# Optimization experiments

Hardware: AMD Instinct MI355X
Metric: run time of the kernel (lower is better)

The kernel has to match this reference:

```python
import jax, jax.numpy as jnp
import numpy as np

BS, N, HD = 16, 96, 128      # batch, nodes per graph, hidden_nf
NL, NS = 4, 2                # n_layers, inv_sublayers
ND, HF = 3, 6                # n_dims, node feature dims (in_node_nf - time)
FIN = HF + 1                 # +1 time channel (condition_time=True)
NF = 100.0                   # normalization_factor, aggregation='sum'


def setup_inputs() -> dict:
    key = jax.random.key(0)
    ks = iter(jax.random.split(key, 40))

    def w(shape, scale=None):
        s = scale if scale is not None else 1.0 / np.sqrt(shape[-2])
        return jax.random.normal(next(ks), shape, jnp.float32) * s

    xh = jax.random.normal(next(ks), (BS, N, ND + HF), jnp.float32)
    t = jnp.array([0.5], jnp.float32)
    nm = (jax.random.uniform(next(ks), (BS, N, 1)) < 0.9).astype(jnp.float32)
    em = nm[:, :, None, :] * nm[:, None, :, :]
    em = em * (1.0 - jnp.eye(N, dtype=jnp.float32)[None, :, :, None])
    G = NL * NS
    return dict(
        xh=xh, t=t, node_mask=nm, edge_mask=em,
        W_emb=w((FIN, HD)), b_emb=jnp.zeros((HD,), jnp.float32),
        gWe1=w((G, 2 * HD + 2, HD)), gbe1=jnp.zeros((G, HD), jnp.float32),
        gWe2=w((G, HD, HD)), gbe2=jnp.zeros((G, HD), jnp.float32),
        gWn1=w((G, 2 * HD, HD)), gbn1=jnp.zeros((G, HD), jnp.float32),
        gWn2=w((G, HD, HD)), gbn2=jnp.zeros((G, HD), jnp.float32),
        eWc1=w((NL, 2 * HD + 2, HD)), ebc1=jnp.zeros((NL, HD), jnp.float32),
        eWc2=w((NL, HD, HD)), ebc2=jnp.zeros((NL, HD), jnp.float32),
        eWc3=w((NL, HD, 1), scale=0.001),   # xavier gain 0.001 as in EDM
        W_out=w((HD, FIN)), b_out=jnp.zeros((FIN,), jnp.float32),
    )


def _pair_mlp(h, ea, W1, b1, W2, b2):
    # silu(Linear(cat([h_i, h_j, ea]))) -> silu(Linear) without materializing the concat
    hi = h @ W1[:HD]            # (B,N,H) source part
    hj = h @ W1[HD:2 * HD]      # (B,N,H) target part
    m = jax.nn.silu(hi[:, :, None, :] + hj[:, None, :, :] + ea @ W1[2 * HD:] + b1)
    return jax.nn.silu(m @ W2 + b2)          # (B,N,N,H)


def _egnn(xh, t, node_mask, edge_mask, W_emb, b_emb, gWe1, gbe1, gWe2, gbe2,
          gWn1, gbn1, gWn2, gbn2, eWc1, ebc1, eWc2, ebc2, eWc3, W_out, b_out):
    xh = xh * node_mask                       # mask padded nodes
    x0 = xh[..., :ND]                         # (B,N,3)
    h_time = jnp.broadcast_to(t.reshape(1, 1, 1), (xh.shape[0], xh.shape[1], 1))
    h = jnp.concatenate([xh[..., ND:], h_time], axis=-1)   # (B,N,FIN)
    h = h @ W_emb + b_emb                     # node embedding
    # initial squared distances (EGNN-level edge_attr, in_edge_nf=1)
    d0 = jnp.sum((x0[:, :, None] - x0[:, None, :]) ** 2, -1, keepdims=True)
    x = x0
    for l in range(NL):                       # EquivariantBlocks
        diff = x[:, :, None] - x[:, None, :]  # x_i - x_j, (B,N,N,3)
        radial = jnp.sum(diff ** 2, -1, keepdims=True)
        coord_diff = diff / jnp.sqrt(radial + 1e-8)   # norm_constant=0
        ea = jnp.concatenate([radial, d0], axis=-1)   # (B,N,N,2)
        for s in range(NS):                   # GCL sublayers
            g = l * NS + s
            m = _pair_mlp(h, ea, gWe1[g], gbe1[g], gWe2[g], gbe2[g]) * edge_mask
            agg = jnp.sum(m, axis=2) / NF     # masked scatter-sum over j onto i
            u = jax.nn.silu(h @ gWn1[g, :HD] + agg @ gWn1[g, HD:] + gbn1[g])
            h = (h + (u @ gWn2[g] + gbn2[g])) * node_mask
        # EquivariantUpdate (tanh=False)
        phi = _pair_mlp(h, ea, eWc1[l], ebc1[l], eWc2[l], ebc2[l])
        trans = coord_diff * (phi @ eWc3[l]) * edge_mask    # (B,N,N,3)
        x = (x + jnp.sum(trans, axis=2) / NF) * node_mask
    h = (h @ W_out + b_out) * node_mask       # embedding_out
    vel = (x - x0) * node_mask
    # remove_mean_with_mask
    n_per = jnp.sum(node_mask, axis=1, keepdims=True)
    vel = vel - (jnp.sum(vel, axis=1, keepdims=True) / n_per) * node_mask
    # drop the appended time channel from h (condition_time=True, context=None)
    return jnp.concatenate([vel, h[..., :HF]], axis=-1)    # (B,N,3+HF)


def reference(xh, t, node_mask, edge_mask, W_emb, b_emb, gWe1, gbe1, gWe2, gbe2,
              gWn1, gbn1, gWn2, gbn2, eWc1, ebc1, eWc2, ebc2, eWc3, W_out, b_out):
    return _egnn(xh, t, node_mask, edge_mask, W_emb, b_emb, gWe1, gbe1, gWe2, gbe2,
                 gWn1, gbn1, gWn2, gbn2, eWc1, ebc1, eWc2, ebc2, eWc3, W_out, b_out)
```

## Files before the change

kernel.cpp:

```cpp
#include <hip/hip_runtime.h>
#include <hip/hip_bf16.h>

#define BSZ 16
#define Nn 96
#define HD 128
#define NDIM 3
#define HFEAT 6
#define FINC 7
#define BN (BSZ*Nn)

typedef const float* fp;
typedef __bf16 bf16x8_t __attribute__((ext_vector_type(8)));
typedef float  f32x4_t  __attribute__((ext_vector_type(4)));

__device__ __forceinline__ float silu(float x){
  float e = __expf(-x);
  return x * __builtin_amdgcn_rcpf(1.f + e);
}
__device__ __forceinline__ unsigned short f2b(float x){
  unsigned u = __float_as_uint(x);
  unsigned r = u + 0x7FFF + ((u>>16)&1);
  return (unsigned short)(r>>16);
}
__device__ __forceinline__ unsigned pkf(float a, float b){
  __hip_bfloat162 h2 = __float22bfloat162_rn(make_float2(a,b));
  return *reinterpret_cast<unsigned*>(&h2);
}


__global__ void k_prep(fp gWe1, fp eWc1, fp gWe2, fp eWc2, fp gWn1, fp gWn2,
                       unsigned short* w1b, unsigned short* w2b,
                       unsigned short* wn1b, unsigned short* wn2b){
  int mid = blockIdx.x;
  if (mid < 12){
    const float* src = (mid<8)? gWe1 + (size_t)mid*258*HD : eWc1 + (size_t)(mid-8)*258*HD;
    unsigned short* dst = w1b + (size_t)mid*32768;
    for (int idx = threadIdx.x; idx < 32768; idx += 256){
      int jj = idx&7, l=(idx>>3)&63, kt=(idx>>9)&3, nt=idx>>11;
      int k = kt*32 + (l>>4)*8 + jj, n = nt*16 + (l&15);
      dst[idx] = f2b(src[(size_t)(k + ((n>>7)<<7))*HD + (n&127)]);
    }
  } else if (mid < 24){
    int m2 = mid-12;
    const float* src = (m2<8)? gWe2 + (size_t)m2*HD*HD : eWc2 + (size_t)(m2-8)*HD*HD;
    unsigned short* dst = w2b + (size_t)m2*HD*HD;
    for (int idx = threadIdx.x; idx < HD*HD; idx += 256){
      int jj = idx&7, l=(idx>>3)&63, kt=(idx>>9)&3, nt=idx>>11;
      int k = kt*32 + (l>>4)*8 + jj, n = nt*16 + (l&15);
      dst[idx] = f2b(src[k*HD+n]);
    }
  } else if (mid < 32){
    int g = mid-24;
    const float* src = gWn1 + (size_t)g*256*HD;
    unsigned short* dst = wn1b + (size_t)g*32768;
    for (int idx = threadIdx.x; idx < 32768; idx += 256){
      int jj = idx&7, l=(idx>>3)&63, kt=(idx>>9)&7, nt=idx>>12;
      int k = kt*32 + (l>>4)*8 + jj, n = nt*16 + (l&15);
      dst[idx] = f2b(src[(size_t)k*HD+n]);
    }
  } else {
    int g = mid-32;
    const float* src = gWn2 + (size_t)g*HD*HD;
    unsigned short* dst = wn2b + (size_t)g*HD*HD;
    for (int idx = threadIdx.x; idx < HD*HD; idx += 256){
      int jj = idx&7, l=(idx>>3)&63, kt=(idx>>9)&3, nt=idx>>11;
      int k = kt*32 + (l>>4)*8 + jj, n = nt*16 + (l&15);
      dst[idx] = f2b(src[k*HD+n]);
    }
  }
}

__global__ void k_embed(fp xh, fp t, fp nm, fp W_emb, fp b_emb,
                        float* h, float* x0, float* xA){
  int bn = blockIdx.x, tid = threadIdx.x;
  float nmv = nm[bn];
  if (tid < NDIM){
    float v = xh[bn*(NDIM+HFEAT)+tid] * nmv;
    x0[bn*3+tid] = v; xA[bn*3+tid] = v;
  }
  float acc = b_emb[tid];
  #pragma unroll
  for (int f=0; f<HFEAT; ++f)
    acc += xh[bn*(NDIM+HFEAT)+NDIM+f] * nmv * W_emb[f*HD+tid];
  acc += t[0] * W_emb[HFEAT*HD+tid];
  h[bn*HD+tid] = acc;
}

__global__ __launch_bounds__(256) void k_hij(const float* hin, const unsigned short* w1m,
                                             fp b1, float* Hi, float* Hj){
  __shared__ unsigned int hf[4*256];
  int tid=threadIdx.x, blk=blockIdx.x;
  int b = blk/6, mt = blk%6;
  int l=tid&63, w=tid>>6;
  { int kp=l, jsub=w;
    int kt=kp>>4, q=(kp>>2)&3, dsub=kp&3;
    int sm = kt + 4*(q&1);
    float2 hv[4];
    #pragma unroll
    for(int r=0;r<4;++r)
      hv[r] = ((const float2*)&hin[(size_t)(b*Nn+mt*16+jsub*4+r)*HD])[kp];
    #pragma unroll
    for(int r=0;r<4;++r){
      int row=jsub*4+r;
      hf[kt*256 + (((row + 16*q) ^ sm)<<2) + dsub] = pkf(hv[r].x,hv[r].y);
    } }
  __syncthreads();
  f32x4_t acc[4];
  #pragma unroll
  for(int s=0;s<4;++s) acc[s]=(f32x4_t){0.f,0.f,0.f,0.f};
  #pragma unroll
  for(int kt=0;kt<4;++kt){
    int pl = l ^ (kt + 4*((l>>4)&1));
    bf16x8_t A = *(const bf16x8_t*)((const unsigned int*)hf + kt*256 + pl*4);
    #pragma unroll
    for(int s=0;s<4;++s){
      bf16x8_t B = *(const bf16x8_t*)(w1m + ((((w*4+s)*4+kt)*64 + l)*8));
      acc[s]=__builtin_amdgcn_mfma_f32_16x16x32_bf16(A, B, acc[s], 0,0,0);
    }
  }
  #pragma unroll
  for(int s=0;s<4;++s){
    int nt=w*4+s, n=nt*16+(l&15);
    float b1v = (nt<8)? b1[n] : 0.f;
    #pragma unroll
    for(int r=0;r<4;++r){
      int R = b*Nn + mt*16 + (l>>4)*4 + r;
      float v = acc[s][r];
      if(nt<8) Hi[(size_t)R*HD+n] = v + b1v;
      else     Hj[(size_t)R*HD+(n-128)] = v;
    }
  }
}

__global__ __launch_bounds__(256,4) void k_pair(const float* Hi, const float* Hj,
    const float* x, const float* x0, fp nm, fp W1f,
    const unsigned short* w2m, fp b2, float* agg){
  __shared__ unsigned int m1f[24*256];
  __shared__ float xs[Nn][3], x0s[Nn][3], nms[Nn], rs[Nn], d0s[Nn];
  __shared__ float red[2][HD];
  int tid=threadIdx.x, bn=blockIdx.x;
  int b=bn/Nn, i=bn%Nn;
  int l=tid&63, w=tid>>6, wm=w>>1, wn=w&1;
  int jg=w;

  for(int idx=tid; idx<Nn*3; idx+=256){ int n=idx/3,d=idx%3;
    xs[n][d]=x[(b*Nn+n)*3+d]; x0s[n][d]=x0[(b*Nn+n)*3+d]; }
  if(tid<Nn) nms[tid]=nm[b*Nn+tid];
  __syncthreads();
  if(tid<Nn){
    float dx0=xs[i][0]-xs[tid][0], dx1=xs[i][1]-xs[tid][1], dx2=xs[i][2]-xs[tid][2];
    rs[tid]=dx0*dx0+dx1*dx1+dx2*dx2;
    float e0=x0s[i][0]-x0s[tid][0], e1=x0s[i][1]-x0s[tid][1], e2=x0s[i][2]-x0s[tid][2];
    d0s[tid]=e0*e0+e1*e1+e2*e2;
  }
  __syncthreads();

  { int kp=l;
    int kt2=kp>>4, q=(kp>>2)&3, dsub=kp&3;
    int sm=kt2+4*(q&1);
    float2 hi=((const float2*)&Hi[(size_t)bn*HD])[kp];
    float2 wr=((const float2*)&W1f[(size_t)(2*HD)*HD])[kp];
    float2 wd=((const float2*)&W1f[(size_t)(2*HD+1)*HD])[kp];
    const float2* HjB=(const float2*)&Hj[(size_t)(b*Nn)*HD];
    #pragma unroll
    for(int half=0; half<2; ++half){
      float2 hjv[12];
      #pragma unroll
      for(int u=0;u<12;++u){
        int rr=half*2+(u/6), mt2=u%6;
        int j=mt2*16+jg*4+rr;
        hjv[u]=HjB[(size_t)j*64+kp];
      }
      #pragma unroll
      for(int u=0;u<12;++u){
        int rr=half*2+(u/6), mt2=u%6;
        int jr=jg*4+rr, j=mt2*16+jr;
        float rv=rs[j], dv=d0s[j];
        float m0 =silu(hi.x+hjv[u].x+rv*wr.x+dv*wd.x);
        float m1v=silu(hi.y+hjv[u].y+rv*wr.y+dv*wd.y);
        m1f[mt2*1024 + kt2*256 + (((jr+16*q)^sm)<<2) + dsub]=pkf(m0,m1v);
      }
    } }
  __syncthreads();

  f32x4_t acc[3][4];
  #pragma unroll
  for(int a=0;a<3;++a)
    #pragma unroll
    for(int s=0;s<4;++s) acc[a][s]=(f32x4_t){0.f,0.f,0.f,0.f};
  #pragma unroll
  for(int kt=0;kt<4;++kt){
    int pl = l ^ (kt + 4*((l>>4)&1));
    bf16x8_t Bk[4];
    #pragma unroll
    for(int s=0;s<4;++s)
      Bk[s] = *(const bf16x8_t*)(w2m + ((((wn*4+s)*4+kt)*64 + l)*8));
    #pragma unroll
    for(int a=0;a<3;++a){
      bf16x8_t A = *(const bf16x8_t*)((const unsigned int*)m1f + (((wm*3+a)*4+kt)*256 + pl*4));
      #pragma unroll
      for(int s=0;s<4;++s)
        acc[a][s]=__builtin_amdgcn_mfma_f32_16x16x32_bf16(A, Bk[s], acc[a][s], 0,0,0);
    }
  }

  float b2v[4], p[4]={0.f,0.f,0.f,0.f};
  #pragma unroll
  for(int s=0;s<4;++s) b2v[s]=b2[(wn*4+s)*16 + (l&15)];
  #pragma unroll
  for(int a=0;a<3;++a)
    #pragma unroll
    for(int r=0;r<4;++r){
      int j=(wm*3+a)*16 + (l>>4)*4 + r;
      float emj=(j==i)?0.f:nms[j];
      #pragma unroll
      for(int s=0;s<4;++s) p[s] += silu(acc[a][s][r]+b2v[s])*emj;
    }
  #pragma unroll
  for(int s=0;s<4;++s){ p[s]+=__shfl_xor(p[s],16); p[s]+=__shfl_xor(p[s],32); }
  if(l<16){
    #pragma unroll
    for(int s=0;s<4;++s) red[wm][wn*64 + s*16 + l]=p[s];
  }
  __syncthreads();
  if(tid<HD) agg[(size_t)bn*HD+tid]=(red[0][tid]+red[1][tid])*nms[i]*(1.f/100.f);
}

__global__ __launch_bounds__(256) void k_nodehij(
    const float* hin, float* hout, const float* agg, fp nm,
    const unsigned short* wn1m, fp bn1v, const unsigned short* wn2m, fp bn2v,
    const unsigned short* w1mA, fp b1A, float* HiA, float* HjA,
    const unsigned short* w1mB, fp b1B, float* HiB, float* HjB){
  __shared__ unsigned int af[8*256];
  __shared__ float fbuf[16*132];
  __shared__ float nmr[16];
  int tid=threadIdx.x, blk=blockIdx.x;
  int b=blk/6, mt=blk%6;
  int R0=b*Nn+mt*16;
  int l=tid&63, w=tid>>6;
  int kp=l, jsub=w;
  int kt0=kp>>4, q=(kp>>2)&3, dsub=kp&3;
  int sm=kt0+4*(q&1);
  if(tid<16) nmr[tid]=nm[R0+tid];
  { float2 hv[4], av[4];
    #pragma unroll
    for(int r=0;r<4;++r){
      hv[r]=((const float2*)&hin[(size_t)(R0+jsub*4+r)*HD])[kp];
      av[r]=((const float2*)&agg[(size_t)(R0+jsub*4+r)*HD])[kp];
    }
    #pragma unroll
    for(int r=0;r<4;++r){
      int row=jsub*4+r;
      unsigned off=(((row+16*q)^sm)<<2)+dsub;
      af[kt0*256+off]=pkf(hv[r].x,hv[r].y);
      af[(4+kt0)*256+off]=pkf(av[r].x,av[r].y);
    } }
  __syncthreads();
  f32x4_t c1[2];
  c1[0]=(f32x4_t){0.f,0.f,0.f,0.f}; c1[1]=(f32x4_t){0.f,0.f,0.f,0.f};
  #pragma unroll
  for(int t=0;t<8;++t){
    int pl = l ^ ((t&3) + 4*((l>>4)&1));
    bf16x8_t A=*(const bf16x8_t*)((const unsigned int*)af + t*256 + pl*4);
    #pragma unroll
    for(int s=0;s<2;++s){
      bf16x8_t B=*(const bf16x8_t*)(wn1m + ((((2*w+s)*8+t)*64+l)*8));
      c1[s]=__builtin_amdgcn_mfma_f32_16x16x32_bf16(A,B,c1[s],0,0,0);
    }
  }
  #pragma unroll
  for(int s=0;s<2;++s){
    int n=(2*w+s)*16+(l&15);
    float bv=bn1v[n];
    #pragma unroll
    for(int r=0;r<4;++r){
      int row=(l>>4)*4+r;
      fbuf[row*132+n]=silu(c1[s][r]+bv);
    }
  }
  __syncthreads();
  #pragma unroll
  for(int r=0;r<4;++r){
    int row=jsub*4+r;
    float2 uv=*(const float2*)&fbuf[row*132+2*kp];
    af[kt0*256 + (((row+16*q)^sm)<<2)+dsub]=pkf(uv.x,uv.y);
  }
  __syncthreads();
  f32x4_t c2[2];
  c2[0]=(f32x4_t){0.f,0.f,0.f,0.f}; c2[1]=(f32x4_t){0.f,0.f,0.f,0.f};
  #pragma unroll
  for(int t=0;t<4;++t){
    int pl = l ^ (t + 4*((l>>4)&1));
    bf16x8_t A=*(const bf16x8_t*)((const unsigned int*)af + t*256 + pl*4);
    #pragma unroll
    for(int s=0;s<2;++s){
      bf16x8_t B=*(const bf16x8_t*)(wn2m + ((((2*w+s)*4+t)*64+l)*8));
      c2[s]=__builtin_amdgcn_mfma_f32_16x16x32_bf16(A,B,c2[s],0,0,0);
    }
  }
  { float hv[2][4];
    #pragma unroll
    for(int s=0;s<2;++s){
      int n=(2*w+s)*16+(l&15);
      #pragma unroll
      for(int r=0;r<4;++r)
        hv[s][r]=hin[(size_t)(R0+(l>>4)*4+r)*HD+n];
    }
    #pragma unroll
    for(int s=0;s<2;++s){
      int n=(2*w+s)*16+(l&15);
      float bv=bn2v[n];
      #pragma unroll
      for(int r=0;r<4;++r){
        int row=(l>>4)*4+r;
        float val=(hv[s][r]+c2[s][r]+bv)*nmr[row];
        hout[(size_t)(R0+row)*HD+n]=val;
        fbuf[row*132+n]=val;
      }
    } }
  __syncthreads();
  #pragma unroll
  for(int r=0;r<4;++r){
    int row=jsub*4+r;
    float2 uv=*(const float2*)&fbuf[row*132+2*kp];
    af[kt0*256 + (((row+16*q)^sm)<<2)+dsub]=pkf(uv.x,uv.y);
  }
  __syncthreads();
  {
    f32x4_t a3[4];
    #pragma unroll
    for(int s=0;s<4;++s) a3[s]=(f32x4_t){0.f,0.f,0.f,0.f};
    #pragma unroll
    for(int t=0;t<4;++t){
      int pl = l ^ (t + 4*((l>>4)&1));
      bf16x8_t A=*(const bf16x8_t*)((const unsigned int*)af + t*256 + pl*4);
      #pragma unroll
      for(int s=0;s<4;++s){
        bf16x8_t B=*(const bf16x8_t*)(w1mA + ((((w*4+s)*4+t)*64+l)*8));
        a3[s]=__builtin_amdgcn_mfma_f32_16x16x32_bf16(A,B,a3[s],0,0,0);
      }
    }
    #pragma unroll
    for(int s=0;s<4;++s){
      int nt=w*4+s, n=nt*16+(l&15);
      float b1v=(nt<8)? b1A[n] : 0.f;
      #pragma unroll
      for(int r=0;r<4;++r){
        int R=R0+(l>>4)*4+r;
        float v=a3[s][r];
        if(nt<8) HiA[(size_t)R*HD+n]=v+b1v;
        else     HjA[(size_t)R*HD+(n-128)]=v;
      }
    }
  }
  if(w1mB){
    f32x4_t a3[4];
    #pragma unroll
    for(int s=0;s<4;++s) a3[s]=(f32x4_t){0.f,0.f,0.f,0.f};
    #pragma unroll
    for(int t=0;t<4;++t){
      int pl = l ^ (t + 4*((l>>4)&1));
      bf16x8_t A=*(const bf16x8_t*)((const unsigned int*)af + t*256 + pl*4);
      #pragma unroll
      for(int s=0;s<4;++s){
        bf16x8_t B=*(const bf16x8_t*)(w1mB + ((((w*4+s)*4+t)*64+l)*8));
        a3[s]=__builtin_amdgcn_mfma_f32_16x16x32_bf16(A,B,a3[s],0,0,0);
      }
    }
    #pragma unroll
    for(int s=0;s<4;++s){
      int nt=w*4+s, n=nt*16+(l&15);
      float b1v=(nt<8)? b1B[n] : 0.f;
      #pragma unroll
      for(int r=0;r<4;++r){
        int R=R0+(l>>4)*4+r;
        float v=a3[s][r];
        if(nt<8) HiB[(size_t)R*HD+n]=v+b1v;
        else     HjB[(size_t)R*HD+(n-128)]=v;
      }
    }
  }
}

__global__ __launch_bounds__(256,4) void k_coord(const float* Hi, const float* Hj,
    const float* x, const float* x0, fp nm, fp W1f,
    const unsigned short* w2m, fp b2, fp W3, float* xn){
  __shared__ unsigned int m1f[24*256];
  __shared__ float xs[Nn][3], x0s[Nn][3], nms[Nn], rs[Nn], d0s[Nn];
  __shared__ float redJ[2][Nn];
  __shared__ float sjs[Nn];
  int tid=threadIdx.x, bn=blockIdx.x;
  int b=bn/Nn, i=bn%Nn;
  int l=tid&63, w=tid>>6, wm=w>>1, wn=w&1;
  int jg=w;

  for(int idx=tid; idx<Nn*3; idx+=256){ int n=idx/3,d=idx%3;
    xs[n][d]=x[(b*Nn+n)*3+d]; x0s[n][d]=x0[(b*Nn+n)*3+d]; }
  if(tid<Nn) nms[tid]=nm[b*Nn+tid];
  __syncthreads();
  if(tid<Nn){
    float dx0=xs[i][0]-xs[tid][0], dx1=xs[i][1]-xs[tid][1], dx2=xs[i][2]-xs[tid][2];
    rs[tid]=dx0*dx0+dx1*dx1+dx2*dx2;
    float e0=x0s[i][0]-x0s[tid][0], e1=x0s[i][1]-x0s[tid][1], e2=x0s[i][2]-x0s[tid][2];
    d0s[tid]=e0*e0+e1*e1+e2*e2;
  }
  __syncthreads();

  { int kp=l;
    int kt2=kp>>4, q=(kp>>2)&3, dsub=kp&3;
    int sm=kt2+4*(q&1);
    float2 hi=((const float2*)&Hi[(size_t)bn*HD])[kp];
    float2 wr=((const float2*)&W1f[(size_t)(2*HD)*HD])[kp];
    float2 wd=((const float2*)&W1f[(size_t)(2*HD+1)*HD])[kp];
    const float2* HjB=(const float2*)&Hj[(size_t)(b*Nn)*HD];
    #pragma unroll
    for(int half=0; half<2; ++half){
      float2 hjv[12];
      #pragma unroll
      for(int u=0;u<12;++u){
        int rr=half*2+(u/6), mt2=u%6;
        int j=mt2*16+jg*4+rr;
        hjv[u]=HjB[(size_t)j*64+kp];
      }
      #pragma unroll
      for(int u=0;u<12;++u){
        int rr=half*2+(u/6), mt2=u%6;
        int jr=jg*4+rr, j=mt2*16+jr;
        float rv=rs[j], dv=d0s[j];
        float m0 =silu(hi.x+hjv[u].x+rv*wr.x+dv*wd.x);
        float m1v=silu(hi.y+hjv[u].y+rv*wr.y+dv*wd.y);
        m1f[mt2*1024 + kt2*256 + (((jr+16*q)^sm)<<2) + dsub]=pkf(m0,m1v);
      }
    } }
  __syncthreads();

  f32x4_t acc[3][4];
  #pragma unroll
  for(int a=0;a<3;++a)
    #pragma unroll
    for(int s=0;s<4;++s) acc[a][s]=(f32x4_t){0.f,0.f,0.f,0.f};
  #pragma unroll
  for(int kt=0;kt<4;++kt){
    int pl = l ^ (kt + 4*((l>>4)&1));
    bf16x8_t Bk[4];
    #pragma unroll
    for(int s=0;s<4;++s)
      Bk[s] = *(const bf16x8_t*)(w2m + ((((wn*4+s)*4+kt)*64 + l)*8));
    #pragma unroll
    for(int a=0;a<3;++a){
      bf16x8_t A = *(const bf16x8_t*)((const unsigned int*)m1f + (((wm*3+a)*4+kt)*256 + pl*4));
      #pragma unroll
      for(int s=0;s<4;++s)
        acc[a][s]=__builtin_amdgcn_mfma_f32_16x16x32_bf16(A, Bk[s], acc[a][s], 0,0,0);
    }
  }

  float b2v[4], w3v[4];
  #pragma unroll
  for(int s=0;s<4;++s){ b2v[s]=b2[(wn*4+s)*16+(l&15)]; w3v[s]=W3[(wn*4+s)*16+(l&15)]; }
  float qv[3][4];
  #pragma unroll
  for(int a=0;a<3;++a)
    #pragma unroll
    for(int r=0;r<4;++r){
      float pj=0.f;
      #pragma unroll
      for(int s=0;s<4;++s) pj += silu(acc[a][s][r]+b2v[s])*w3v[s];
      qv[a][r]=pj;
    }
  #pragma unroll
  for(int d=1;d<16;d<<=1)
    #pragma unroll
    for(int a=0;a<3;++a)
      #pragma unroll
      for(int r=0;r<4;++r)
        qv[a][r] += __shfl_xor(qv[a][r], d);
  if((l&15)==0){
    int quad=l>>4;
    #pragma unroll
    for(int a=0;a<3;++a)
      #pragma unroll
      for(int r=0;r<4;++r)
        redJ[wn][(wm*3+a)*16 + quad*4 + r]=qv[a][r];
  }
  __syncthreads();
  if(tid<Nn){
    float pj=redJ[0][tid]+redJ[1][tid];
    float em=(tid==i)?0.f:nms[tid];
    sjs[tid]=pj*em*rsqrtf(rs[tid]+1e-8f);
  }
  __syncthreads();
  if(w<3){
    int d=w;
    float xi=xs[i][d];
    float s=(xi-xs[l][d])*sjs[l];
    if(l<32) s += (xi-xs[l+64][d])*sjs[l+64];
    s+=__shfl_xor(s,1); s+=__shfl_xor(s,2); s+=__shfl_xor(s,4);
    s+=__shfl_xor(s,8); s+=__shfl_xor(s,16); s+=__shfl_xor(s,32);
    if(l==0) xn[(size_t)(b*Nn+i)*3+d]=(xi+s*(1.f/100.f))*nms[i];
  }
}

__global__ void k_velstat(const float* xf, const float* x0, fp nm, float* vstat){
  __shared__ float sh[128];
  int b=blockIdx.x, tid=threadIdx.x;
  float nmv = (tid<Nn)? nm[b*Nn+tid] : 0.f;
  float vals[4];
  #pragma unroll
  for(int d=0;d<3;++d)
    vals[d] = (tid<Nn)? (xf[(b*Nn+tid)*3+d]-x0[(b*Nn+tid)*3+d])*nmv : 0.f;
  vals[3]=nmv;
  #pragma unroll
  for(int q=0;q<4;++q){
    sh[tid]=vals[q]; __syncthreads();
    for(int s=64;s>0;s>>=1){ if(tid<s) sh[tid]+=sh[tid+s]; __syncthreads(); }
    if(tid==0) vstat[b*4+q]=sh[0];
    __syncthreads();
  }
}

__global__ void k_out(const float* h, const float* xf, const float* x0, fp nm,
                      const float* vstat, fp W_out, fp b_out, float* out){
  __shared__ float shh[HD];
  int bn=blockIdx.x, tid=threadIdx.x, b=bn/Nn;
  shh[tid]=h[bn*HD+tid]; __syncthreads();
  float nmv=nm[bn];
  if(tid<3){
    float vel=(xf[bn*3+tid]-x0[bn*3+tid])*nmv;
    float mean=vstat[b*4+tid]/vstat[b*4+3];
    out[bn*(NDIM+HFEAT)+tid]=vel-mean*nmv;
  } else if(tid<3+HFEAT){
    int f=tid-3;
    float acc=b_out[f];
    for(int k=0;k<HD;++k) acc+=shh[k]*W_out[k*FINC+f];
    out[bn*(NDIM+HFEAT)+tid]=acc*nmv;
  }
}

extern "C" void kernel_launch(void* const* d_in, const int* in_sizes, int n_in,
                              void* d_out, int out_size, void* d_ws, size_t ws_size,
                              hipStream_t stream) {
  fp xh   =(fp)d_in[0];
  fp t    =(fp)d_in[1];
  fp nm   =(fp)d_in[2];
  fp W_emb=(fp)d_in[4],  b_emb=(fp)d_in[5];
  fp gWe1 =(fp)d_in[6],  gbe1 =(fp)d_in[7];
  fp gWe2 =(fp)d_in[8],  gbe2 =(fp)d_in[9];
  fp gWn1 =(fp)d_in[10], gbn1 =(fp)d_in[11];
  fp gWn2 =(fp)d_in[12], gbn2 =(fp)d_in[13];
  fp eWc1 =(fp)d_in[14], ebc1 =(fp)d_in[15];
  fp eWc2 =(fp)d_in[16], ebc2 =(fp)d_in[17];
  fp eWc3 =(fp)d_in[18];
  fp W_out=(fp)d_in[19], b_out=(fp)d_in[20];

  unsigned short* w1b  = (unsigned short*)d_ws;
  unsigned short* w2b  = w1b  + (size_t)12*32768;
  unsigned short* wn1b = w2b  + (size_t)12*16384;
  unsigned short* wn2b = wn1b + (size_t)8*32768;
  float* fbase = (float*)(wn2b + (size_t)8*16384);
  float* hA   = fbase;
  float* hB   = hA  + BN*HD;
  float* HiA  = hB  + BN*HD;
  float* HjA  = HiA + BN*HD;
  float* HiE  = HjA + BN*HD;
  float* HjE  = HiE + BN*HD;
  float* agg  = HjE + BN*HD;
  float* x0   = agg + BN*HD;
  float* xA   = x0  + BN*3;
  float* xB   = xA  + BN*3;
  float* vstat= xB  + BN*3;

  k_prep <<<40,256,0,stream>>>(gWe1, eWc1, gWe2, eWc2, gWn1, gWn2, w1b, w2b, wn1b, wn2b);
  k_embed<<<BN,128,0,stream>>>(xh,t,nm,W_emb,b_emb,hA,x0,xA);
  k_hij  <<<96,256,0,stream>>>(hA, w1b, gbe1, HiA, HjA);
  float *hc=hA, *hn=hB, *xc=xA, *xn=xB;
  for(int l=0;l<4;++l){
    int g=2*l;
    k_pair<<<BN,256,0,stream>>>(HiA,HjA,xc,x0,nm, gWe1+(size_t)g*258*HD,
          w2b+(size_t)g*HD*HD, gbe2+(size_t)g*HD, agg);
    k_nodehij<<<96,256,0,stream>>>(hc,hn,agg,nm,
          wn1b+(size_t)g*32768, gbn1+(size_t)g*HD,
          wn2b+(size_t)g*16384, gbn2+(size_t)g*HD,
          w1b+(size_t)(g+1)*32768, gbe1+(size_t)(g+1)*HD, HiA, HjA,
          nullptr, nullptr, nullptr, nullptr);
    { float* tmp=hc; hc=hn; hn=tmp; }
    g=2*l+1;
    k_pair<<<BN,256,0,stream>>>(HiA,HjA,xc,x0,nm, gWe1+(size_t)g*258*HD,
          w2b+(size_t)g*HD*HD, gbe2+(size_t)g*HD, agg);
    bool last = (l==3);
    k_nodehij<<<96,256,0,stream>>>(hc,hn,agg,nm,
          wn1b+(size_t)g*32768, gbn1+(size_t)g*HD,
          wn2b+(size_t)g*16384, gbn2+(size_t)g*HD,
          w1b+(size_t)(8+l)*32768, ebc1+(size_t)l*HD, HiE, HjE,
          last? nullptr : w1b+(size_t)(g+1)*32768,
          last? nullptr : gbe1+(size_t)(g+1)*HD, HiA, HjA);
    { float* tmp=hc; hc=hn; hn=tmp; }
    k_coord<<<BN,256,0,stream>>>(HiE,HjE,xc,x0,nm, eWc1+(size_t)l*258*HD,
          w2b+(size_t)(8+l)*HD*HD, ebc2+(size_t)l*HD,
          eWc3+(size_t)l*HD, xn);
    { float* tmp=xc; xc=xn; xn=tmp; }
  }
  k_velstat<<<BSZ,128,0,stream>>>(xc,x0,nm,vstat);
  k_out   <<<BN,128,0,stream>>>(hc,xc,x0,nm,vstat,W_out,b_out,(float*)d_out);
}
```

Baseline: 430.6 us.

## Fuse pair aggregation and node update via last-block atomic counter

Merges the pair-message kernel and the node-update/Hi-Hj projection kernel into one launch. Each block bumps an atomic counter for its 16-row tile, and the last block to finish runs the node MLP for those rows. This removes a kernel launch and the global barrier between the two stages per sublayer. Hi/Hj buffers are double-buffered (HiC/HjC) so a tile's next-layer projections cannot overwrite inputs other blocks are still reading. The x/x0 shared-memory staging is also replaced with direct global loads for distances. The cost is a serialized tail on the last block per tile and reliance on the ordering of atomic release/acquire.

```diff
diff --git a/kernel.cpp b/kernel.cpp
--- a/kernel.cpp
+++ b/kernel.cpp
@@ -30,7 +30,7 @@
 
 __global__ void k_prep(fp gWe1, fp eWc1, fp gWe2, fp eWc2, fp gWn1, fp gWn2,
                        unsigned short* w1b, unsigned short* w2b,
-                       unsigned short* wn1b, unsigned short* wn2b){
+                       unsigned short* wn1b, unsigned short* wn2b, int* ctr){
   int mid = blockIdx.x;
   if (mid < 12){
     const float* src = (mid<8)? gWe1 + (size_t)mid*258*HD : eWc1 + (size_t)(mid-8)*258*HD;
@@ -58,7 +58,7 @@
       int k = kt*32 + (l>>4)*8 + jj, n = nt*16 + (l&15);
       dst[idx] = f2b(src[(size_t)k*HD+n]);
     }
-  } else {
+  } else if (mid < 40){
     int g = mid-32;
     const float* src = gWn2 + (size_t)g*HD*HD;
     unsigned short* dst = wn2b + (size_t)g*HD*HD;
@@ -67,6 +67,8 @@
       int k = kt*32 + (l>>4)*8 + jj, n = nt*16 + (l&15);
       dst[idx] = f2b(src[k*HD+n]);
     }
+  } else {
+    for (int idx = threadIdx.x; idx < 8*96; idx += 256) ctr[idx]=0;
   }
 }
 
@@ -132,26 +134,38 @@
   }
 }
 
-__global__ __launch_bounds__(256,4) void k_pair(const float* Hi, const float* Hj,
+__global__ __launch_bounds__(256,4) void k_pairnode(const float* Hi, const float* Hj,
+    const float* hin, float* hout,
     const float* x, const float* x0, fp nm, fp W1f,
-    const unsigned short* w2m, fp b2, float* agg){
-  __shared__ unsigned int m1f[24*256];
-  __shared__ float xs[Nn][3], x0s[Nn][3], nms[Nn], rs[Nn], d0s[Nn];
-  __shared__ float red[2][HD];
+    const unsigned short* w2m, fp b2, float* agg, int* ctr,
+    const unsigned short* wn1m, fp bn1v, const unsigned short* wn2m, fp bn2v,
+    const unsigned short* w1mA, fp b1A, float* HiA, float* HjA,
+    const unsigned short* w1mB, fp b1B, float* HiB, float* HjB){
+  __shared__ union {
+    struct {
+      unsigned int m1f[24*256];
+      float nms[Nn], rs[Nn], d0s[Nn];
+      float red[2][HD];
+    } P;
+    struct {
+      unsigned int af[8*256];
+      float fbuf[16*132];
+      float nmr[16];
+    } N;
+  } U;
+  __shared__ int isLast;
   int tid=threadIdx.x, bn=blockIdx.x;
   int b=bn/Nn, i=bn%Nn;
   int l=tid&63, w=tid>>6, wm=w>>1, wn=w&1;
   int jg=w;
 
-  for(int idx=tid; idx<Nn*3; idx+=256){ int n=idx/3,d=idx%3;
-    xs[n][d]=x[(b*Nn+n)*3+d]; x0s[n][d]=x0[(b*Nn+n)*3+d]; }
-  if(tid<Nn) nms[tid]=nm[b*Nn+tid];
-  __syncthreads();
   if(tid<Nn){
-    float dx0=xs[i][0]-xs[tid][0], dx1=xs[i][1]-xs[tid][1], dx2=xs[i][2]-xs[tid][2];
-    rs[tid]=dx0*dx0+dx1*dx1+dx2*dx2;
-    float e0=x0s[i][0]-x0s[tid][0], e1=x0s[i][1]-x0s[tid][1], e2=x0s[i][2]-x0s[tid][2];
-    d0s[tid]=e0*e0+e1*e1+e2*e2;
+    int jj=b*Nn+tid, ii=b*Nn+i;
+    float dx0=x[ii*3]-x[jj*3], dx1=x[ii*3+1]-x[jj*3+1], dx2=x[ii*3+2]-x[jj*3+2];
+    U.P.rs[tid]=dx0*dx0+dx1*dx1+dx2*dx2;
+    float e0=x0[ii*3]-x0[jj*3], e1=x0[ii*3+1]-x0[jj*3+1], e2=x0[ii*3+2]-x0[jj*3+2];
+    U.P.d0s[tid]=e0*e0+e1*e1+e2*e2;
+    U.P.nms[tid]=nm[jj];
   }
   __syncthreads();
 
@@ -161,7 +175,7 @@
     float2 hi=((const float2*)&Hi[(size_t)bn*HD])[kp];
     float2 wr=((const float2*)&W1f[(size_t)(2*HD)*HD])[kp];
     float2 wd=((const float2*)&W1f[(size_t)(2*HD+1)*HD])[kp];
-    const float2* HjB=(const float2*)&Hj[(size_t)(b*Nn)*HD];
+    const float2* HjB2=(const float2*)&Hj[(size_t)(b*Nn)*HD];
     #pragma unroll
     for(int half=0; half<2; ++half){
       float2 hjv[12];
@@ -169,16 +183,16 @@
       for(int u=0;u<12;++u){
         int rr=half*2+(u/6), mt2=u%6;
         int j=mt2*16+jg*4+rr;
-        hjv[u]=HjB[(size_t)j*64+kp];
+        hjv[u]=HjB2[(size_t)j*64+kp];
       }
       #pragma unroll
       for(int u=0;u<12;++u){
         int rr=half*2+(u/6), mt2=u%6;
         int jr=jg*4+rr, j=mt2*16+jr;
-        float rv=rs[j], dv=d0s[j];
+        float rv=U.P.rs[j], dv=U.P.d0s[j];
         float m0 =silu(hi.x+hjv[u].x+rv*wr.x+dv*wd.x);
         float m1v=silu(hi.y+hjv[u].y+rv*wr.y+dv*wd.y);
-        m1f[mt2*1024 + kt2*256 + (((jr+16*q)^sm)<<2) + dsub]=pkf(m0,m1v);
+        U.P.m1f[mt2*1024 + kt2*256 + (((jr+16*q)^sm)<<2) + dsub]=pkf(m0,m1v);
       }
     } }
   __syncthreads();
@@ -197,7 +211,7 @@
       Bk[s] = *(const bf16x8_t*)(w2m + ((((wn*4+s)*4+kt)*64 + l)*8));
     #pragma unroll
     for(int a=0;a<3;++a){
-      bf16x8_t A = *(const bf16x8_t*)((const unsigned int*)m1f + (((wm*3+a)*4+kt)*256 + pl*4));
+      bf16x8_t A = *(const bf16x8_t*)((const unsigned int*)U.P.m1f + (((wm*3+a)*4+kt)*256 + pl*4));
       #pragma unroll
       for(int s=0;s<4;++s)
         acc[a][s]=__builtin_amdgcn_mfma_f32_16x16x32_bf16(A, Bk[s], acc[a][s], 0,0,0);
@@ -212,7 +226,7 @@
     #pragma unroll
     for(int r=0;r<4;++r){
       int j=(wm*3+a)*16 + (l>>4)*4 + r;
-      float emj=(j==i)?0.f:nms[j];
+      float emj=(j==i)?0.f:U.P.nms[j];
       #pragma unroll
       for(int s=0;s<4;++s) p[s] += silu(acc[a][s][r]+b2v[s])*emj;
     }
@@ -220,163 +234,163 @@
   for(int s=0;s<4;++s){ p[s]+=__shfl_xor(p[s],16); p[s]+=__shfl_xor(p[s],32); }
   if(l<16){
     #pragma unroll
-    for(int s=0;s<4;++s) red[wm][wn*64 + s*16 + l]=p[s];
-  }
-  __syncthreads();
-  if(tid<HD) agg[(size_t)bn*HD+tid]=(red[0][tid]+red[1][tid])*nms[i]*(1.f/100.f);
-}
-
-__global__ __launch_bounds__(256) void k_nodehij(
-    const float* hin, float* hout, const float* agg, fp nm,
-    const unsigned short* wn1m, fp bn1v, const unsigned short* wn2m, fp bn2v,
-    const unsigned short* w1mA, fp b1A, float* HiA, float* HjA,
-    const unsigned short* w1mB, fp b1B, float* HiB, float* HjB){
-  __shared__ unsigned int af[8*256];
-  __shared__ float fbuf[16*132];
-  __shared__ float nmr[16];
-  int tid=threadIdx.x, blk=blockIdx.x;
-  int b=blk/6, mt=blk%6;
-  int R0=b*Nn+mt*16;
-  int l=tid&63, w=tid>>6;
-  int kp=l, jsub=w;
-  int kt0=kp>>4, q=(kp>>2)&3, dsub=kp&3;
-  int sm=kt0+4*(q&1);
-  if(tid<16) nmr[tid]=nm[R0+tid];
-  { float2 hv[4], av[4];
-    #pragma unroll
-    for(int r=0;r<4;++r){
-      hv[r]=((const float2*)&hin[(size_t)(R0+jsub*4+r)*HD])[kp];
-      av[r]=((const float2*)&agg[(size_t)(R0+jsub*4+r)*HD])[kp];
-    }
+    for(int s=0;s<4;++s) U.P.red[wm][wn*64 + s*16 + l]=p[s];
+  }
+  __syncthreads();
+  if(tid<HD){
+    float v=(U.P.red[0][tid]+U.P.red[1][tid])*U.P.nms[i]*(1.f/100.f);
+    __hip_atomic_store(&agg[(size_t)bn*HD+tid], v, __ATOMIC_RELAXED, __HIP_MEMORY_SCOPE_AGENT);
+  }
+  __syncthreads();
+  if(tid==0){
+    int old=__hip_atomic_fetch_add(&ctr[bn>>4],1,__ATOMIC_ACQ_REL,__HIP_MEMORY_SCOPE_AGENT);
+    isLast=(old==15);
+  }
+  __syncthreads();
+  if(!isLast) return;
+
+  {
+    int R0 = bn & ~15;
+    int kp=l, jsub=w;
+    int kt0=kp>>4, q=(kp>>2)&3, dsub=kp&3;
+    int sm=kt0+4*(q&1);
+    if(tid<16) U.N.nmr[tid]=nm[R0+tid];
+    { float2 hv[4], av[4];
+      #pragma unroll
+      for(int r=0;r<4;++r){
+        hv[r]=((const float2*)&hin[(size_t)(R0+jsub*4+r)*HD])[kp];
+        av[r]=((const float2*)&agg[(size_t)(R0+jsub*4+r)*HD])[kp];
+      }
+      #pragma unroll
+      for(int r=0;r<4;++r){
+        int row=jsub*4+r;
+        unsigned off=(((row+16*q)^sm)<<2)+dsub;
+        U.N.af[kt0*256+off]=pkf(hv[r].x,hv[r].y);
+        U.N.af[(4+kt0)*256+off]=pkf(av[r].x,av[r].y);
+      } }
+    __syncthreads();
+    f32x4_t c1[2];
+    c1[0]=(f32x4_t){0.f,0.f,0.f,0.f}; c1[1]=(f32x4_t){0.f,0.f,0.f,0.f};
+    #pragma unroll
+    for(int t=0;t<8;++t){
+      int pl = l ^ ((t&3) + 4*((l>>4)&1));
+      bf16x8_t A=*(const bf16x8_t*)((const unsigned int*)U.N.af + t*256 + pl*4);
+      #pragma unroll
+      for(int s=0;s<2;++s){
+        bf16x8_t B=*(const bf16x8_t*)(wn1m + ((((2*w+s)*8+t)*64+l)*8));
+        c1[s]=__builtin_amdgcn_mfma_f32_16x16x32_bf16(A,B,c1[s],0,0,0);
+      }
+    }
+    #pragma unroll
+    for(int s=0;s<2;++s){
+      int n=(2*w+s)*16+(l&15);
+      float bv=bn1v[n];
+      #pragma unroll
+      for(int r=0;r<4;++r){
+        int row=(l>>4)*4+r;
+        U.N.fbuf[row*132+n]=silu(c1[s][r]+bv);
+      }
+    }
+    __syncthreads();
     #pragma unroll
     for(int r=0;r<4;++r){
       int row=jsub*4+r;
-      unsigned off=(((row+16*q)^sm)<<2)+dsub;
-      af[kt0*256+off]=pkf(hv[r].x,hv[r].y);
-      af[(4+kt0)*256+off]=pkf(av[r].x,av[r].y);
-    } }
-  __syncthreads();
-  f32x4_t c1[2];
-  c1[0]=(f32x4_t){0.f,0.f,0.f,0.f}; c1[1]=(f32x4_t){0.f,0.f,0.f,0.f};
-  #pragma unroll
-  for(int t=0;t<8;++t){
-    int pl = l ^ ((t&3) + 4*((l>>4)&1));
-    bf16x8_t A=*(const bf16x8_t*)((const unsigned int*)af + t*256 + pl*4);
-    #pragma unroll
-    for(int s=0;s<2;++s){
-      bf16x8_t B=*(const bf16x8_t*)(wn1m + ((((2*w+s)*8+t)*64+l)*8));
-      c1[s]=__builtin_amdgcn_mfma_f32_16x16x32_bf16(A,B,c1[s],0,0,0);
-    }
-  }
-  #pragma unroll
-  for(int s=0;s<2;++s){
-    int n=(2*w+s)*16+(l&15);
-    float bv=bn1v[n];
-    #pragma unroll
-    for(int r=0;r<4;++r){
-      int row=(l>>4)*4+r;
-      fbuf[row*132+n]=silu(c1[s][r]+bv);
-    }
-  }
-  __syncthreads();
-  #pragma unroll
-  for(int r=0;r<4;++r){
-    int row=jsub*4+r;
-    float2 uv=*(const float2*)&fbuf[row*132+2*kp];
-    af[kt0*256 + (((row+16*q)^sm)<<2)+dsub]=pkf(uv.x,uv.y);
-  }
-  __syncthreads();
-  f32x4_t c2[2];
-  c2[0]=(f32x4_t){0.f,0.f,0.f,0.f}; c2[1]=(f32x4_t){0.f,0.f,0.f,0.f};
-  #pragma unroll
-  for(int t=0;t<4;++t){
-    int pl = l ^ (t + 4*((l>>4)&1));
-    bf16x8_t A=*(const bf16x8_t*)((const unsigned int*)af + t*256 + pl*4);
-    #pragma unroll
-    for(int s=0;s<2;++s){
-      bf16x8_t B=*(const bf16x8_t*)(wn2m + ((((2*w+s)*4+t)*64+l)*8));
-      c2[s]=__builtin_amdgcn_mfma_f32_16x16x32_bf16(A,B,c2[s],0,0,0);
-    }
-  }
-  { float hv[2][4];
-    #pragma unroll
-    for(int s=0;s<2;++s){
-      int n=(2*w+s)*16+(l&15);
-      #pragma unroll
-      for(int r=0;r<4;++r)
-        hv[s][r]=hin[(size_t)(R0+(l>>4)*4+r)*HD+n];
-    }
-    #pragma unroll
-    for(int s=0;s<2;++s){
-      int n=(2*w+s)*16+(l&15);
-      float bv=bn2v[n];
-      #pragma unroll
-      for(int r=0;r<4;++r){
-        int row=(l>>4)*4+r;
-        float val=(hv[s][r]+c2[s][r]+bv)*nmr[row];
-        hout[(size_t)(R0+row)*HD+n]=val;
-        fbuf[row*132+n]=val;
-      }
-    } }
-  __syncthreads();
-  #pragma unroll
-  for(int r=0;r<4;++r){
-    int row=jsub*4+r;
-    float2 uv=*(const float2*)&fbuf[row*132+2*kp];
-    af[kt0*256 + (((row+16*q)^sm)<<2)+dsub]=pkf(uv.x,uv.y);
-  }
-  __syncthreads();
-  {
-    f32x4_t a3[4];
-    #pragma unroll
-    for(int s=0;s<4;++s) a3[s]=(f32x4_t){0.f,0.f,0.f,0.f};
+      float2 uv=*(const float2*)&U.N.fbuf[row*132+2*kp];
+      U.N.af[kt0*256 + (((row+16*q)^sm)<<2)+dsub]=pkf(uv.x,uv.y);
+    }
+    __syncthreads();
+    f32x4_t c2[2];
+    c2[0]=(f32x4_t){0.f,0.f,0.f,0.f}; c2[1]=(f32x4_t){0.f,0.f,0.f,0.f};
     #pragma unroll
     for(int t=0;t<4;++t){
       int pl = l ^ (t + 4*((l>>4)&1));
-      bf16x8_t A=*(const bf16x8_t*)((const unsigned int*)af + t*256 + pl*4);
+      bf16x8_t A=*(const bf16x8_t*)((const unsigned int*)U.N.af + t*256 + pl*4);
+      #pragma unroll
+      for(int s=0;s<2;++s){
+        bf16x8_t B=*(const bf16x8_t*)(wn2m + ((((2*w+s)*4+t)*64+l)*8));
+        c2[s]=__builtin_amdgcn_mfma_f32_16x16x32_bf16(A,B,c2[s],0,0,0);
+      }
+    }
+    { float hv[2][4];
+      #pragma unroll
+      for(int s=0;s<2;++s){
+        int n=(2*w+s)*16+(l&15);
+        #pragma unroll
+        for(int r=0;r<4;++r)
+          hv[s][r]=hin[(size_t)(R0+(l>>4)*4+r)*HD+n];
+      }
+      #pragma unroll
+      for(int s=0;s<2;++s){
+        int n=(2*w+s)*16+(l&15);
+        float bv=bn2v[n];
+        #pragma unroll
+        for(int r=0;r<4;++r){
+          int row=(l>>4)*4+r;
+          float val=(hv[s][r]+c2[s][r]+bv)*U.N.nmr[row];
+          hout[(size_t)(R0+row)*HD+n]=val;
+          U.N.fbuf[row*132+n]=val;
+        }
+      } }
+    __syncthreads();
+    #pragma unroll
+    for(int r=0;r<4;++r){
+      int row=jsub*4+r;
+      float2 uv=*(const float2*)&U.N.fbuf[row*132+2*kp];
+      U.N.af[kt0*256 + (((row+16*q)^sm)<<2)+dsub]=pkf(uv.x,uv.y);
+    }
+    __syncthreads();
+    {
+      f32x4_t a3[4];
+      #pragma unroll
+      for(int s=0;s<4;++s) a3[s]=(f32x4_t){0.f,0.f,0.f,0.f};
+      #pragma unroll
+      for(int t=0;t<4;++t){
+        int pl = l ^ (t + 4*((l>>4)&1));
+        bf16x8_t A=*(const bf16x8_t*)((const unsigned int*)U.N.af + t*256 + pl*4);
+        #pragma unroll
+        for(int s=0;s<4;++s){
+          bf16x8_t B=*(const bf16x8_t*)(w1mA + ((((w*4+s)*4+t)*64+l)*8));
+          a3[s]=__builtin_amdgcn_mfma_f32_16x16x32_bf16(A,B,a3[s],0,0,0);
+        }
+      }
       #pragma unroll
       for(int s=0;s<4;++s){
-        bf16x8_t B=*(const bf16x8_t*)(w1mA + ((((w*4+s)*4+t)*64+l)*8));
-        a3[s]=__builtin_amdgcn_mfma_f32_16x16x32_bf16(A,B,a3[s],0,0,0);
-      }
-    }
-    #pragma unroll
-    for(int s=0;s<4;++s){
-      int nt=w*4+s, n=nt*16+(l&15);
-      float b1v=(nt<8)? b1A[n] : 0.f;
-      #pragma unroll
-      for(int r=0;r<4;++r){
-        int R=R0+(l>>4)*4+r;
-        float v=a3[s][r];
-        if(nt<8) HiA[(size_t)R*HD+n]=v+b1v;
-        else     HjA[(size_t)R*HD+(n-128)]=v;
-      }
-    }
-  }
-  if(w1mB){
-    f32x4_t a3[4];
-    #pragma unroll
-    for(int s=0;s<4;++s) a3[s]=(f32x4_t){0.f,0.f,0.f,0.f};
-    #pragma unroll
-    for(int t=0;t<4;++t){
-      int pl = l ^ (t + 4*((l>>4)&1));
-      bf16x8_t A=*(const bf16x8_t*)((const unsigned int*)af + t*256 + pl*4);
+        int nt=w*4+s, n=nt*16+(l&15);
+        float b1v=(nt<8)? b1A[n] : 0.f;
+        #pragma unroll
+        for(int r=0;r<4;++r){
+          int R=R0+(l>>4)*4+r;
+          float v=a3[s][r];
+          if(nt<8) HiA[(size_t)R*HD+n]=v+b1v;
+          else     HjA[(size_t)R*HD+(n-128)]=v;
+        }
+      }
+    }
+    if(w1mB){
+      f32x4_t a3[4];
+      #pragma unroll
+      for(int s=0;s<4;++s) a3[s]=(f32x4_t){0.f,0.f,0.f,0.f};
+      #pragma unroll
+      for(int t=0;t<4;++t){
+        int pl = l ^ (t + 4*((l>>4)&1));
+        bf16x8_t A=*(const bf16x8_t*)((const unsigned int*)U.N.af + t*256 + pl*4);
+        #pragma unroll
+        for(int s=0;s<4;++s){
+          bf16x8_t B=*(const bf16x8_t*)(w1mB + ((((w*4+s)*4+t)*64+l)*8));
+          a3[s]=__builtin_amdgcn_mfma_f32_16x16x32_bf16(A,B,a3[s],0,0,0);
+        }
+      }
       #pragma unroll
       for(int s=0;s<4;++s){
-        bf16x8_t B=*(const bf16x8_t*)(w1mB + ((((w*4+s)*4+t)*64+l)*8));
-        a3[s]=__builtin_amdgcn_mfma_f32_16x16x32_bf16(A,B,a3[s],0,0,0);
-      }
-    }
-    #pragma unroll
-    for(int s=0;s<4;++s){
-      int nt=w*4+s, n=nt*16+(l&15);
-      float b1v=(nt<8)? b1B[n] : 0.f;
-      #pragma unroll
-      for(int r=0;r<4;++r){
-        int R=R0+(l>>4)*4+r;
-        float v=a3[s][r];
-        if(nt<8) HiB[(size_t)R*HD+n]=v+b1v;
-        else     HjB[(size_t)R*HD+(n-128)]=v;
+        int nt=w*4+s, n=nt*16+(l&15);
+        float b1v=(nt<8)? b1B[n] : 0.f;
+        #pragma unroll
+        for(int r=0;r<4;++r){
+          int R=R0+(l>>4)*4+r;
+          float v=a3[s][r];
+          if(nt<8) HiB[(size_t)R*HD+n]=v+b1v;
+          else     HjB[(size_t)R*HD+(n-128)]=v;
+        }
       }
     }
   }
@@ -386,7 +400,7 @@
     const float* x, const float* x0, fp nm, fp W1f,
     const unsigned short* w2m, fp b2, fp W3, float* xn){
   __shared__ unsigned int m1f[24*256];
-  __shared__ float xs[Nn][3], x0s[Nn][3], nms[Nn], rs[Nn], d0s[Nn];
+  __shared__ float xs[Nn][3], nms[Nn], rs[Nn], d0s[Nn];
   __shared__ float redJ[2][Nn];
   __shared__ float sjs[Nn];
   int tid=threadIdx.x, bn=blockIdx.x;
@@ -394,16 +408,16 @@
   int l=tid&63, w=tid>>6, wm=w>>1, wn=w&1;
   int jg=w;
 
+  if(tid<Nn){
+    int jj=b*Nn+tid, ii=b*Nn+i;
+    float dx0=x[ii*3]-x[jj*3], dx1=x[ii*3+1]-x[jj*3+1], dx2=x[ii*3+2]-x[jj*3+2];
+    rs[tid]=dx0*dx0+dx1*dx1+dx2*dx2;
+    float e0=x0[ii*3]-x0[jj*3], e1=x0[ii*3+1]-x0[jj*3+1], e2=x0[ii*3+2]-x0[jj*3+2];
+    d0s[tid]=e0*e0+e1*e1+e2*e2;
+    nms[tid]=nm[jj];
+  }
   for(int idx=tid; idx<Nn*3; idx+=256){ int n=idx/3,d=idx%3;
-    xs[n][d]=x[(b*Nn+n)*3+d]; x0s[n][d]=x0[(b*Nn+n)*3+d]; }
-  if(tid<Nn) nms[tid]=nm[b*Nn+tid];
-  __syncthreads();
-  if(tid<Nn){
-    float dx0=xs[i][0]-xs[tid][0], dx1=xs[i][1]-xs[tid][1], dx2=xs[i][2]-xs[tid][2];
-    rs[tid]=dx0*dx0+dx1*dx1+dx2*dx2;
-    float e0=x0s[i][0]-x0s[tid][0], e1=x0s[i][1]-x0s[tid][1], e2=x0s[i][2]-x0s[tid][2];
-    d0s[tid]=e0*e0+e1*e1+e2*e2;
-  }
+    xs[n][d]=x[(b*Nn+n)*3+d]; }
   __syncthreads();
 
   { int kp=l;
@@ -557,12 +571,15 @@
   unsigned short* w2b  = w1b  + (size_t)12*32768;
   unsigned short* wn1b = w2b  + (size_t)12*16384;
   unsigned short* wn2b = wn1b + (size_t)8*32768;
-  float* fbase = (float*)(wn2b + (size_t)8*16384);
+  int*   ctr  = (int*)(wn2b + (size_t)8*16384);
+  float* fbase = (float*)(ctr + 8*96);
   float* hA   = fbase;
   float* hB   = hA  + BN*HD;
   float* HiA  = hB  + BN*HD;
   float* HjA  = HiA + BN*HD;
-  float* HiE  = HjA + BN*HD;
+  float* HiC  = HjA + BN*HD;
+  float* HjC  = HiC + BN*HD;
+  float* HiE  = HjC + BN*HD;
   float* HjE  = HiE + BN*HD;
   float* agg  = HjE + BN*HD;
   float* x0   = agg + BN*HD;
@@ -570,25 +587,23 @@
   float* xB   = xA  + BN*3;
   float* vstat= xB  + BN*3;
 
-  k_prep <<<40,256,0,stream>>>(gWe1, eWc1, gWe2, eWc2, gWn1, gWn2, w1b, w2b, wn1b, wn2b);
+  k_prep <<<41,256,0,stream>>>(gWe1, eWc1, gWe2, eWc2, gWn1, gWn2, w1b, w2b, wn1b, wn2b, ctr);
   k_embed<<<BN,128,0,stream>>>(xh,t,nm,W_emb,b_emb,hA,x0,xA);
   k_hij  <<<96,256,0,stream>>>(hA, w1b, gbe1, HiA, HjA);
   float *hc=hA, *hn=hB, *xc=xA, *xn=xB;
   for(int l=0;l<4;++l){
     int g=2*l;
-    k_pair<<<BN,256,0,stream>>>(HiA,HjA,xc,x0,nm, gWe1+(size_t)g*258*HD,
-          w2b+(size_t)g*HD*HD, gbe2+(size_t)g*HD, agg);
-    k_nodehij<<<96,256,0,stream>>>(hc,hn,agg,nm,
+    k_pairnode<<<BN,256,0,stream>>>(HiA,HjA, hc,hn, xc,x0,nm, gWe1+(size_t)g*258*HD,
+          w2b+(size_t)g*HD*HD, gbe2+(size_t)g*HD, agg, ctr+g*96,
           wn1b+(size_t)g*32768, gbn1+(size_t)g*HD,
           wn2b+(size_t)g*16384, gbn2+(size_t)g*HD,
-          w1b+(size_t)(g+1)*32768, gbe1+(size_t)(g+1)*HD, HiA, HjA,
+          w1b+(size_t)(g+1)*32768, gbe1+(size_t)(g+1)*HD, HiC, HjC,
           nullptr, nullptr, nullptr, nullptr);
     { float* tmp=hc; hc=hn; hn=tmp; }
     g=2*l+1;
-    k_pair<<<BN,256,0,stream>>>(HiA,HjA,xc,x0,nm, gWe1+(size_t)g*258*HD,
-          w2b+(size_t)g*HD*HD, gbe2+(size_t)g*HD, agg);
     bool last = (l==3);
-    k_nodehij<<<96,256,0,stream>>>(hc,hn,agg,nm,
+    k_pairnode<<<BN,256,0,stream>>>(HiC,HjC, hc,hn, xc,x0,nm, gWe1+(size_t)g*258*HD,
+          w2b+(size_t)g*HD*HD, gbe2+(size_t)g*HD, agg, ctr+g*96,
           wn1b+(size_t)g*32768, gbn1+(size_t)g*HD,
           wn2b+(size_t)g*16384, gbn2+(size_t)g*HD,
           w1b+(size_t)(8+l)*32768, ebc1+(size_t)l*HD, HiE, HjE,
```

After: 668.0 us. 1.55x slower.
